# Optimization experiments

Measured on AMD Instinct MI355X. Metric: run time of the kernel, lower is better.

The kernel has to match this reference:

```python
import jax, jax.numpy as jnp
import numpy as np

N, C, H, W = 8, 256, 52, 52
N_WIN, NUM_HEADS, TOPK = 7, 1, 4
RS = (H // N_WIN, W // N_WIN)  # region size (7, 7)
SCALE = C ** -0.5


def _avg_pool_ceil(t):
    # F.avg_pool2d(kernel=RS, stride=RS, ceil_mode=True, count_include_pad=False)
    B, Ch, h_in, w_in = t.shape
    h = -(-h_in // RS[0]); w = -(-w_in // RS[1])
    tp = jnp.pad(t, ((0, 0), (0, 0), (0, h * RS[0] - h_in), (0, w * RS[1] - w_in)))
    s = tp.reshape(B, Ch, h, RS[0], w, RS[1]).sum(axis=(3, 5))
    rc = np.minimum(RS[0], h_in - np.arange(h) * RS[0]).astype(np.float32)
    cc = np.minimum(RS[1], w_in - np.arange(w) * RS[1]).astype(np.float32)
    return s / (rc[:, None] * cc[None, :])


def _nearest_up(t):
    # F.interpolate(mode='nearest', scale_factor=RS) for integer scales == repeat
    return jnp.repeat(jnp.repeat(t, RS[0], axis=2), RS[1], axis=3)


def _grid2seq(t):
    # BCHW -> (B, nhead, nregion, reg_area, head_dim)
    B, Ch, Hp, Wp = t.shape
    rh, rw = Hp // RS[0], Wp // RS[1]
    hd = Ch // NUM_HEADS
    t = t.reshape(B, NUM_HEADS, hd, rh, RS[0], rw, RS[1]).transpose(0, 1, 3, 5, 4, 6, 2)
    return t.reshape(B, NUM_HEADS, rh * rw, RS[0] * RS[1], hd), rh, rw


def _forward(x, y, q_w, q_b, k_w, k_b):
    q = jnp.einsum('nchw,oc->nohw', x, q_w) + q_b[None, :, None, None]
    k = jnp.einsum('nchw,oc->nohw', y, k_w) + k_b[None, :, None, None]
    # routing path uses detached q, k
    q_r = _avg_pool_ceil(jax.lax.stop_gradient(q))  # (B, C, 8, 8)
    k_r = _avg_pool_ceil(jax.lax.stop_gradient(k))
    B, _, h, w = q_r.shape
    nreg = h * w
    a_r = jnp.einsum('nchw,ncyx->nhwyx', q_r, k_r).reshape(B, nreg, nreg)
    idx = jax.lax.top_k(a_r, TOPK)[1]                              # (B, nreg, topk)
    idx = jnp.broadcast_to(idx[:, None], (B, NUM_HEADS, nreg, TOPK))
    a_r = SCALE * a_r
    # coarse scores upsampled over key pixels, then over query pixels
    a1 = _nearest_up(a_r.reshape(B, nreg, h, w))                   # (B, nreg, Hp, Wp)
    Hp, Wp = a1.shape[2], a1.shape[3]
    a1 = _nearest_up(a1.transpose(0, 2, 3, 1).reshape(B, Hp * Wp, h, w))  # (B, Hp*Wp, Hp, Wp)
    reg_area = (Hp * Wp) // nreg
    a6 = a1.reshape(B, NUM_HEADS, nreg, reg_area // NUM_HEADS, nreg, reg_area)
    # fine attention on padded q, k
    pad_b = (RS[0] - H % RS[0]) % RS[0]
    pad_r = (RS[1] - W % RS[1]) % RS[1]
    qp = jnp.pad(q, ((0, 0), (0, 0), (0, pad_b), (0, pad_r)))
    kp = jnp.pad(k, ((0, 0), (0, 0), (0, pad_b), (0, pad_r)))
    q_seq, rh, rw = _grid2seq(qp)   # (B, nh, nreg, reg_area, hd)
    k_seq, _, _ = _grid2seq(kp)
    bI = jnp.arange(B)[:, None, None, None]
    mI = jnp.arange(NUM_HEADS)[None, :, None, None]
    key_g = k_seq[bI, mI, idx]      # gather top-k key regions: (B, nh, nreg, topk, reg_area, hd)
    attn = jnp.einsum('bmrqd,bmrtkd->bmrqtk', q_seq * SCALE, key_g)
    # torch.scatter along dim 4 with index repeated over the t' axis -> duplicate
    # writes to the same slot; serial torch scatter keeps the LAST write (t'=TOPK-1)
    vals = attn[:, :, :, :TOPK, TOPK - 1, :]  # (B, nh, nreg, topk, reg_area)
    rI = jnp.arange(nreg)[None, None, :, None]
    tI = jnp.arange(TOPK)[None, None, None, :]
    corr = a6.at[bI, mI, rI, tI, idx].set(vals)
    # _corr2grid: 10-dim view + 'bmhwpqyxcd->bmhpwqycxd'
    c10 = corr.reshape(B, NUM_HEADS, rh, rw, RS[0], RS[1], rh, rw, RS[0], RS[1])
    c10 = c10.transpose(0, 1, 2, 4, 3, 5, 6, 8, 7, 9)
    Hf, Wf = rh * RS[0], rw * RS[1]
    corr = c10.reshape(B, NUM_HEADS, Hf, Wf, Hf, Wf)
    corr = corr[:, :, :Hf - pad_b, :Wf - pad_r, :Hf - pad_b, :Wf - pad_r]
    return corr.transpose(0, 2, 3, 1, 4, 5)  # (B, H, W, nhead, H, W)


def setup_inputs():
    ks = jax.random.split(jax.random.key(0), 6)
    return {
        'x': jax.random.normal(ks[0], (N, C, H, W), jnp.float32),
        'y': jax.random.normal(ks[1], (N, C, H, W), jnp.float32),
        'q_w': jax.random.normal(ks[2], (C, C), jnp.float32) * (C ** -0.5),
        'q_b': jax.random.normal(ks[3], (C,), jnp.float32) * 0.02,
        'k_w': jax.random.normal(ks[4], (C, C), jnp.float32) * (C ** -0.5),
        'k_b': jax.random.normal(ks[5], (C,), jnp.float32) * 0.02,
    }


def reference(x, y, q_w, q_b, k_w, k_b):
    return _forward(x, y, q_w, q_b, k_w, k_b)
```

## Files before the change

### kernel.cpp

```cpp
#include <hip/hip_runtime.h>

#define NB 8
#define C 256
#define HW 52
#define P (HW*HW)
#define NREG 64
#define NTOPK 4
#define SCALE 0.0625f

static __device__ __forceinline__ int d7(int v)  { return (v*9363) >> 16; }
static __device__ __forceinline__ int d56(int v) { return (v*18725) >> 20; }
static __device__ __forceinline__ int d13(int v) { return (v*10083) >> 17; }

__global__ __launch_bounds__(256) void k1_pool_prep(
    const float* __restrict__ x, const float* __restrict__ y,
    const float* __restrict__ qw, const float* __restrict__ qb,
    const float* __restrict__ kw, const float* __restrict__ kb,
    float* __restrict__ xr, float* __restrict__ yr, float* __restrict__ xg,
    float* __restrict__ M, float* __restrict__ u, float* __restrict__ v2,
    float* __restrict__ c0p)
{
    __shared__ float sm[4*P];
    const int tid = threadIdx.x;

    if (blockIdx.x >= 1024) {
        const int pb = blockIdx.x - 1024;
        if (pb == 64) {
            float ua = 0.f, va = 0.f;
            for (int e = 0; e < 256; e++) {
                ua += qb[e] * kw[e*256 + tid];
                va += kb[e] * qw[e*256 + tid];
            }
            u[tid] = ua; v2[tid] = va;
            if (tid == 0) {
                float c = 0.f;
                for (int e = 0; e < 256; e++) c += qb[e]*kb[e];
                c0p[0] = c;
            }
            return;
        }
        const int cx0 = pb * 4;
        float (*wqs)[4] = (float(*)[4])sm;
        *(float4*)&wqs[tid][0] = *(const float4*)(qw + tid*256 + cx0);
        __syncthreads();
        float a0=0.f, a1=0.f, a2=0.f, a3=0.f;
        #pragma unroll 4
        for (int o = 0; o < 256; o++) {
            const float wk = kw[o*256 + tid];
            const float4 wq = *(const float4*)&wqs[o][0];
            a0 += wq.x*wk; a1 += wq.y*wk; a2 += wq.z*wk; a3 += wq.w*wk;
        }
        M[(cx0+0)*256 + tid] = a0;
        M[(cx0+1)*256 + tid] = a1;
        M[(cx0+2)*256 + tid] = a2;
        M[(cx0+3)*256 + tid] = a3;
        return;
    }

    const int w = tid >> 6, lane = tid & 63;
    const int pl = blockIdx.x*4 + w;
    const int proj = pl >> 11;
    const int bcid = pl & 2047;
    const float* src = (proj ? y : x) + (size_t)bcid * P;
    float* plane = sm + w*P;
    {
        const float4* s4 = (const float4*)src;
        float4* p4 = (float4*)plane;
        for (int g = lane; g < 676; g += 64) p4[g] = s4[g];
    }
    __syncthreads();
    const int jh = lane >> 3, jw = lane & 7;
    const int y0 = jh*7, x0 = jw*7;
    const int ry = min(7, HW - y0), rx = min(7, HW - x0);
    float s = 0.f;
    for (int dy = 0; dy < ry; ++dy) {
        const float* row = plane + (y0 + dy)*HW + x0;
        for (int dx = 0; dx < rx; ++dx) s += row[dx];
    }
    (proj ? yr : xr)[bcid*64 + lane] = s / (float)(ry*rx);
    if (!proj) {
        const float* r0 = plane + y0*HW + x0;
        float4 g4;
        g4.x = r0[0]; g4.y = r0[1]; g4.z = r0[2];
        g4.w = (x0 + 3 < HW) ? r0[3] : 0.f;
        *(float4*)&xg[bcid*256 + lane*4] = g4;
    }
}

__global__ __launch_bounds__(256) void k2_gemms(
    const float* __restrict__ xr, const float* __restrict__ yr,
    const float* __restrict__ qw, const float* __restrict__ qb,
    const float* __restrict__ kw, const float* __restrict__ kb,
    float* __restrict__ qr, float* __restrict__ kr,
    const float* __restrict__ xg, const float* __restrict__ M,
    const float* __restrict__ u, float* __restrict__ G)
{
    __shared__ float As[32][64];
    __shared__ float Bs[32][64];
    const int tid = threadIdx.x;
    const int tx = tid & 15, ty = tid >> 4;

    float acc[4][4];
    #pragma unroll
    for (int i = 0; i < 4; i++)
        #pragma unroll
        for (int j = 0; j < 4; j++) acc[i][j] = 0.f;

    if (blockIdx.x < 64) {
        const int bp = blockIdx.x >> 2;
        const int b = bp >> 1, proj = bp & 1;
        const float* X = (proj ? yr : xr) + b*C*64;
        const float* W = proj ? kw : qw;
        const float* Bv = proj ? kb : qb;
        float* O = (proj ? kr : qr) + b*C*64;
        const int o0 = (blockIdx.x & 3) * 64;

        const int aor = tid & 63;
        const int akc = (tid >> 6) * 8;
        const int bkr = tid >> 3;
        const int bjc = (tid & 7) * 8;

        for (int k0 = 0; k0 < 256; k0 += 32) {
            const float4 w0 = *(const float4*)(W + (o0 + aor)*256 + k0 + akc);
            const float4 w1 = *(const float4*)(W + (o0 + aor)*256 + k0 + akc + 4);
            const float4 x0v = *(const float4*)(X + (k0 + bkr)*64 + bjc);
            const float4 x1v = *(const float4*)(X + (k0 + bkr)*64 + bjc + 4);
            __syncthreads();
            As[akc+0][aor] = w0.x; As[akc+1][aor] = w0.y; As[akc+2][aor] = w0.z; As[akc+3][aor] = w0.w;
            As[akc+4][aor] = w1.x; As[akc+5][aor] = w1.y; As[akc+6][aor] = w1.z; As[akc+7][aor] = w1.w;
            *(float4*)&Bs[bkr][bjc] = x0v;
            *(float4*)&Bs[bkr][bjc+4] = x1v;
            __syncthreads();
            #pragma unroll
            for (int kk = 0; kk < 32; kk++) {
                const float4 a = *(const float4*)&As[kk][ty*4];
                const float4 bb = *(const float4*)&Bs[kk][tx*4];
                const float av[4] = {a.x, a.y, a.z, a.w};
                const float bv[4] = {bb.x, bb.y, bb.z, bb.w};
                #pragma unroll
                for (int i = 0; i < 4; i++)
                    #pragma unroll
                    for (int j = 0; j < 4; j++) acc[i][j] += av[i]*bv[j];
            }
        }
        #pragma unroll
        for (int i = 0; i < 4; i++) {
            const int o = o0 + ty*4 + i;
            const float bias = Bv[o];
            float4 ov;
            ov.x = acc[i][0]+bias; ov.y = acc[i][1]+bias;
            ov.z = acc[i][2]+bias; ov.w = acc[i][3]+bias;
            *(float4*)(O + o*64 + tx*4) = ov;
        }
    } else {
        const int id2 = blockIdx.x - 64;
        const int b = id2 >> 4, sub = id2 & 15;
        const int p0 = (sub >> 2)*64, o0 = (sub & 3)*64;
        const float* Xg = xg + b*C*256;
        float* Gb = G + b*256*256;

        const int lkr = tid >> 3;
        const int ljc = (tid & 7) * 8;

        for (int k0 = 0; k0 < 256; k0 += 32) {
            const float4 a0 = *(const float4*)(Xg + (k0 + lkr)*256 + p0 + ljc);
            const float4 a1 = *(const float4*)(Xg + (k0 + lkr)*256 + p0 + ljc + 4);
            const float4 b0 = *(const float4*)(M + (k0 + lkr)*256 + o0 + ljc);
            const float4 b1 = *(const float4*)(M + (k0 + lkr)*256 + o0 + ljc + 4);
            __syncthreads();
            *(float4*)&As[lkr][ljc] = a0; *(float4*)&As[lkr][ljc+4] = a1;
            *(float4*)&Bs[lkr][ljc] = b0; *(float4*)&Bs[lkr][ljc+4] = b1;
            __syncthreads();
            #pragma unroll
            for (int kk = 0; kk < 32; kk++) {
                const float4 a = *(const float4*)&As[kk][ty*4];
                const float4 bb = *(const float4*)&Bs[kk][tx*4];
                const float av[4] = {a.x, a.y, a.z, a.w};
                const float bv[4] = {bb.x, bb.y, bb.z, bb.w};
                #pragma unroll
                for (int i = 0; i < 4; i++)
                    #pragma unroll
                    for (int j = 0; j < 4; j++) acc[i][j] += av[i]*bv[j];
            }
        }
        const float4 u4 = *(const float4*)(u + o0 + tx*4);
        #pragma unroll
        for (int i = 0; i < 4; i++) {
            float4 ov;
            ov.x = acc[i][0]+u4.x; ov.y = acc[i][1]+u4.y;
            ov.z = acc[i][2]+u4.z; ov.w = acc[i][3]+u4.w;
            *(float4*)(Gb + (p0 + ty*4 + i)*256 + o0 + tx*4) = ov;
        }
    }
}

__global__ __launch_bounds__(256) void k3_topk_vals(
    const float* __restrict__ y, const float* __restrict__ qr,
    const float* __restrict__ kr, const float* __restrict__ G,
    const float* __restrict__ xg, const float* __restrict__ v2,
    const float* __restrict__ c0p,
    float* __restrict__ arT, int* __restrict__ idxout, float* __restrict__ vals)
{
    const int b = blockIdx.y, r = blockIdx.x;
    __shared__ float pdot[4][64];
    __shared__ float Gs[4][256];
    __shared__ float Hs[4];
    __shared__ int gsh;
    __shared__ float Ys[49][260];
    const int tid = threadIdx.x, w = tid >> 6, lane = tid & 63;

    {
        const float* qcol = qr + b*C*64 + r;
        const float* kcol = kr + b*C*64 + lane;
        float d = 0.f;
        #pragma unroll 8
        for (int cc = 0; cc < 64; cc++) {
            const int c = w*64 + cc;
            d += qcol[c*64] * kcol[c*64];
        }
        pdot[w][lane] = d;
    }
    *(float4*)&Gs[w][lane*4] = *(const float4*)(G + ((b*256 + r*4 + w)*256) + lane*4);
    {
        const int pos = r*4 + w;
        float acc = 0.f;
        #pragma unroll
        for (int cc = 0; cc < 4; cc++) {
            const int c = lane + cc*64;
            acc += xg[(b*256 + c)*256 + pos] * v2[c];
        }
        #pragma unroll
        for (int off = 32; off >= 1; off >>= 1) acc += __shfl_xor(acc, off);
        if (lane == 0) Hs[w] = acc + c0p[0];
    }
    __syncthreads();

    if (w == 0) {
        const float dot = pdot[0][lane] + pdot[1][lane] + pdot[2][lane] + pdot[3][lane];
        arT[(b*64 + lane)*64 + r] = dot * SCALE;
        float v = dot;
        const int my = lane;
        #pragma unroll
        for (int t = 0; t < NTOPK; t++) {
            float bv = v; int bi = my;
            #pragma unroll
            for (int off = 32; off >= 1; off >>= 1) {
                const float ov = __shfl_xor(bv, off);
                const int   oi = __shfl_xor(bi, off);
                if (ov > bv || (ov == bv && oi < bi)) { bv = ov; bi = oi; }
            }
            if (lane == 0) {
                idxout[(b*64 + r)*NTOPK + t] = bi;
                if (t == NTOPK-1) gsh = bi;
            }
            if (my == bi) v = -3.0e38f;
        }
    }
    __syncthreads();

    const int g = gsh;
    const int gy = g >> 3, gx = g & 7;
    if (tid < 245) {
        const int c5 = tid / 49, k2 = tid % 49;
        const int dy = d7(k2), dx = k2 - dy*7;
        const int kY = gy*7 + dy, kX = gx*7 + dx;
        const bool ok = (kY < HW) && (kX < HW);
        const float* srcp = y + (size_t)(b*256)*P + kY*HW + kX;
        for (int c = c5; c < 256; c += 5)
            Ys[k2][c] = ok ? srcp[(size_t)c*P] : 0.f;
    }
    __syncthreads();

    if (tid < NTOPK*49) {
        const int t = tid / 49, k2 = tid % 49;
        const int qX = (r & 7)*7 + t;
        const int dy = d7(k2), dx = k2 - dy*7;
        const int kY = gy*7 + dy, kX = gx*7 + dx;
        float res = 0.f;
        if (qX < HW && kY < HW && kX < HW) {
            const float4* Gp = (const float4*)&Gs[t][0];
            const float4* Yp = (const float4*)&Ys[k2][0];
            float dot = 0.f;
            #pragma unroll 8
            for (int cc = 0; cc < 64; cc++) {
                const float4 a = Gp[cc], yy = Yp[cc];
                dot += a.x*yy.x + a.y*yy.y + a.z*yy.z + a.w*yy.w;
            }
            res = SCALE * (dot + Hs[t]);
        }
        vals[((b*64 + r)*NTOPK + t)*49 + k2] = res;
    }
}

__global__ __launch_bounds__(256) void fill_kernel(
    const float* __restrict__ arT, const float* __restrict__ vals,
    const int* __restrict__ idx, float* __restrict__ out)
{
    const int b = blockIdx.y;
    const int yx = blockIdx.x;
    const int Y1 = yx / HW, X1 = yx % HW;
    const int r1 = (Y1/7)*8 + X1/7;
    const int q1 = (Y1%7)*7 + X1%7;
    const int p2 = r1*49 + q1;
    const int yy = p2/56, xx = p2 - 56*yy;
    const int regB = (yy/7)*8 + xx/7;

    __shared__ float acol[64];
    __shared__ float vrow[49];
    const int tid = threadIdx.x;
    if (tid < 64) acol[tid] = arT[(b*64 + regB)*64 + tid];
    int ovr = -1;
    if (q1 < NTOPK) {
        ovr = idx[(b*64 + r1)*NTOPK + q1];
        if (tid < 49) vrow[tid] = vals[((b*64 + r1)*NTOPK + q1)*49 + tid];
    }
    __syncthreads();

    float* plane = out + (size_t)(b*P + yx) * P;
    for (int u = tid; u < 676; u += 256) {
        const int Y2 = d13(u);
        const int g4 = u - Y2*13;
        const int X2b = g4*4;
        const int ry2 = d7(Y2);
        const int my2 = Y2 - ry2*7;
        float res[4];
        #pragma unroll
        for (int j = 0; j < 4; j++) {
            const int X2 = X2b + j;
            const int rx2 = d7(X2);
            const int mx2 = X2 - rx2*7;
            const int r2 = ry2*8 + rx2;
            const int k2 = my2*7 + mx2;
            const int P1 = r2*49 + k2;
            const int Yp = d56(P1);
            const int Xp = P1 - Yp*56;
            const int regA = d7(Yp)*8 + d7(Xp);
            float v = acol[regA];
            if (r2 == ovr) v = vrow[k2];
            res[j] = v;
        }
        float4 o; o.x = res[0]; o.y = res[1]; o.z = res[2]; o.w = res[3];
        *(float4*)(plane + Y2*HW + X2b) = o;
    }
}

extern "C" void kernel_launch(void* const* d_in, const int* in_sizes, int n_in,
                              void* d_out, int out_size, void* d_ws, size_t ws_size,
                              hipStream_t stream)
{
    const float* x  = (const float*)d_in[0];
    const float* y  = (const float*)d_in[1];
    const float* qw = (const float*)d_in[2];
    const float* qb = (const float*)d_in[3];
    const float* kw = (const float*)d_in[4];
    const float* kb = (const float*)d_in[5];
    float* out = (float*)d_out;

    float* xr  = out;
    float* yr  = xr + 131072;
    float* qr  = yr + 131072;
    float* kr  = qr + 131072;
    float* xg  = kr + 131072;
    float* G   = xg + 524288;
    float* M   = G  + 524288;
    float* u   = M  + 65536;
    float* v2  = u  + 256;
    float* c0p = v2 + 256;

    float* ws  = (float*)d_ws;
    float* arT = ws;
    float* vls = arT + 32768;
    int*   idx = (int*)(vls + 100352);

    k1_pool_prep<<<1089, 256, 0, stream>>>(x, y, qw, qb, kw, kb, xr, yr, xg, M, u, v2, c0p);
    k2_gemms<<<192, 256, 0, stream>>>(xr, yr, qw, qb, kw, kb, qr, kr, xg, M, u, G);
    k3_topk_vals<<<dim3(64, 8), 256, 0, stream>>>(y, qr, kr, G, xg, v2, c0p, arT, idx, vls);
    fill_kernel<<<dim3(P, 8), 256, 0, stream>>>(arT, vls, idx, out);
}
```

Before: 115.9 us.

## Transpose y to channel-last so top-k gather reads coalesced float4 rows

Adds extra blocks to the first kernel that transpose y into a pixel-major, channel-contiguous scratch buffer (yT) through a padded shared-memory tile. The top-k kernel then fills its key-region tile with contiguous float4 loads per pixel, instead of per-channel scalar loads strided by a whole plane. This targets the uncoalesced gather in k3. The cost is an extra full read and write of y in k1. The scratch sits in the output buffer, which the fill kernel later overwrites.

```diff
diff --git a/kernel.cpp b/kernel.cpp
--- a/kernel.cpp
+++ b/kernel.cpp
@@ -12,19 +12,58 @@
 static __device__ __forceinline__ int d56(int v) { return (v*18725) >> 20; }
 static __device__ __forceinline__ int d13(int v) { return (v*10083) >> 17; }
 
-__global__ __launch_bounds__(256) void k1_pool_prep(
+__global__ __launch_bounds__(256) void k1_pool_prep_tr(
     const float* __restrict__ x, const float* __restrict__ y,
     const float* __restrict__ qw, const float* __restrict__ qb,
     const float* __restrict__ kw, const float* __restrict__ kb,
     float* __restrict__ xr, float* __restrict__ yr, float* __restrict__ xg,
     float* __restrict__ M, float* __restrict__ u, float* __restrict__ v2,
-    float* __restrict__ c0p)
+    float* __restrict__ c0p, float* __restrict__ yT)
 {
     __shared__ float sm[4*P];
     const int tid = threadIdx.x;
-
-    if (blockIdx.x >= 1024) {
-        const int pb = blockIdx.x - 1024;
+    const int bx = blockIdx.x;
+
+    if (bx >= 1089) {
+        const int tb = bx - 1089;
+        const int b = tb / 172;
+        const int rem = tb - b*172;
+        const int ct = rem / 43;
+        const int pt = rem - ct*43;
+        const int c0 = ct*64, pos0 = pt*64;
+        float* tile = sm;
+        const float* ysrc = y + ((size_t)(b*256 + c0))*P;
+        #pragma unroll
+        for (int p = 0; p < 4; p++) {
+            const int cr = p*16 + (tid>>4);
+            const int f4 = tid&15;
+            const int pos = pos0 + f4*4;
+            if (pos < P) {
+                const float4 v = *(const float4*)(ysrc + (size_t)cr*P + pos);
+                float* d = tile + cr*65 + f4*4;
+                d[0]=v.x; d[1]=v.y; d[2]=v.z; d[3]=v.w;
+            }
+        }
+        __syncthreads();
+        #pragma unroll
+        for (int p = 0; p < 4; p++) {
+            const int pj = p*16 + (tid>>4);
+            const int c4 = tid&15;
+            const int pos = pos0 + pj;
+            if (pos < P) {
+                float4 v;
+                v.x = tile[(c4*4+0)*65 + pj];
+                v.y = tile[(c4*4+1)*65 + pj];
+                v.z = tile[(c4*4+2)*65 + pj];
+                v.w = tile[(c4*4+3)*65 + pj];
+                *(float4*)(yT + ((size_t)(b*P + pos))*256 + c0 + c4*4) = v;
+            }
+        }
+        return;
+    }
+
+    if (bx >= 1024) {
+        const int pb = bx - 1024;
         if (pb == 64) {
             float ua = 0.f, va = 0.f;
             for (int e = 0; e < 256; e++) {
@@ -58,7 +97,7 @@
     }
 
     const int w = tid >> 6, lane = tid & 63;
-    const int pl = blockIdx.x*4 + w;
+    const int pl = bx*4 + w;
     const int proj = pl >> 11;
     const int bcid = pl & 2047;
     const float* src = (proj ? y : x) + (size_t)bcid * P;
@@ -195,7 +234,7 @@
 }
 
 __global__ __launch_bounds__(256) void k3_topk_vals(
-    const float* __restrict__ y, const float* __restrict__ qr,
+    const float* __restrict__ yT, const float* __restrict__ qr,
     const float* __restrict__ kr, const float* __restrict__ G,
     const float* __restrict__ xg, const float* __restrict__ v2,
     const float* __restrict__ c0p,
@@ -260,14 +299,14 @@
 
     const int g = gsh;
     const int gy = g >> 3, gx = g & 7;
-    if (tid < 245) {
-        const int c5 = tid / 49, k2 = tid % 49;
+    for (int i = tid; i < 49*64; i += 256) {
+        const int k2 = i >> 6, f4 = i & 63;
         const int dy = d7(k2), dx = k2 - dy*7;
         const int kY = gy*7 + dy, kX = gx*7 + dx;
-        const bool ok = (kY < HW) && (kX < HW);
-        const float* srcp = y + (size_t)(b*256)*P + kY*HW + kX;
-        for (int c = c5; c < 256; c += 5)
-            Ys[k2][c] = ok ? srcp[(size_t)c*P] : 0.f;
+        float4 v = make_float4(0.f, 0.f, 0.f, 0.f);
+        if (kY < HW && kX < HW)
+            v = *(const float4*)(yT + ((size_t)(b*P + kY*HW + kX))*256 + f4*4);
+        *(float4*)&Ys[k2][f4*4] = v;
     }
     __syncthreads();
 
@@ -366,14 +405,16 @@
     float* u   = M  + 65536;
     float* v2  = u  + 256;
     float* c0p = v2 + 256;
+    float* yT  = c0p + 16;
 
     float* ws  = (float*)d_ws;
     float* arT = ws;
     float* vls = arT + 32768;
     int*   idx = (int*)(vls + 100352);
 
-    k1_pool_prep<<<1089, 256, 0, stream>>>(x, y, qw, qb, kw, kb, xr, yr, xg, M, u, v2, c0p);
+    k1_pool_prep_tr<<<2465, 256, 0, stream>>>(x, y, qw, qb, kw, kb, xr, yr, xg,
+                                              M, u, v2, c0p, yT);
     k2_gemms<<<192, 256, 0, stream>>>(xr, yr, qw, qb, kw, kb, qr, kr, xg, M, u, G);
-    k3_topk_vals<<<dim3(64, 8), 256, 0, stream>>>(y, qr, kr, G, xg, v2, c0p, arT, idx, vls);
+    k3_topk_vals<<<dim3(64, 8), 256, 0, stream>>>(yT, qr, kr, G, xg, v2, c0p, arT, idx, vls);
     fill_kernel<<<dim3(P, 8), 256, 0, stream>>>(arT, vls, idx, out);
 }
```

Result: faster. 112.6 us (-2.9%).
